# Optimization experiments

Measured on AMD Instinct MI355X. Metric: run time of the kernel, lower is better.

The kernel has to match this reference:

```python
import jax, jax.numpy as jnp
import numpy as np

# Sizes (see shape_source): node irreps 32x0e + 16x1o, edge SH 1x1o,
# messages after concat/filter = 48x0e + 48x1o, MLP 16->64->64->96,
# final equivariant Linear -> 32x0e + 16x1o.
N, E = 50000, 800000
S_IN, V_IN, INV = 32, 16, 16
S_MSG, V_MSG = S_IN + V_IN, S_IN + V_IN  # 48, 48
NFAC = S_MSG + V_MSG                      # 96
S_OUT, V_OUT = 32, 16
SQRT3 = 3.0 ** 0.5


def setup_inputs() -> dict:
    key = jax.random.key(0)
    ks = jax.random.split(key, 12)
    return {
        "edge_src": jax.random.randint(ks[0], (E,), 0, N),
        "edge_dst": jax.random.randint(ks[1], (E,), 0, N),
        "edge_weight_cutoff": jax.random.uniform(ks[2], (E,), dtype=jnp.float32),
        "edge_inv": jax.random.normal(ks[3], (E, INV), dtype=jnp.float32),
        "node_scalars": jax.random.normal(ks[4], (N, S_IN), dtype=jnp.float32),
        "node_vectors": jax.random.normal(ks[5], (N, V_IN, 3), dtype=jnp.float32),
        "edge_sh_vec": jax.random.normal(ks[6], (E, 1, 3), dtype=jnp.float32),
        "W0": jax.random.normal(ks[7], (INV, 64), dtype=jnp.float32),
        "W1": jax.random.normal(ks[8], (64, 64), dtype=jnp.float32),
        "W2": jax.random.normal(ks[9], (64, NFAC), dtype=jnp.float32),
        "WL_s": jax.random.normal(ks[10], (S_MSG, S_OUT), dtype=jnp.float32),
        "WL_v": jax.random.normal(ks[11], (V_MSG, V_OUT), dtype=jnp.float32),
    }


def reference(edge_src, edge_dst, edge_weight_cutoff, edge_inv,
              node_scalars, node_vectors, edge_sh_vec,
              W0, W1, W2, WL_s, WL_v):
    # gather source-node features per edge
    src_s = node_scalars[edge_src]            # [E, 32]
    src_v = node_vectors[edge_src]            # [E, 16, 3]
    ev = edge_sh_vec[:, 0, :]                 # [E, 3] equivariant edge vector (1o)

    # equivariant tensor product (component-normalized CG paths):
    #   0e x 1o -> 1o : scalar * vector
    tp_v = src_s[:, :, None] * edge_sh_vec    # [E, 32, 3]
    #   1o x 1o -> 0e : dot / sqrt(3)   (1e, 2e outputs dropped by the output-irreps filter)
    tp_s = jnp.einsum('eci,ei->ec', src_v, ev) / SQRT3  # [E, 16]

    # concatenate with gathered node features and regroup by irrep
    msg_s = jnp.concatenate([tp_s, src_s], axis=-1)     # [E, 48] (0e block)
    msg_v = jnp.concatenate([tp_v, src_v], axis=1)      # [E, 48, 3] (1o block)

    # edge-conditioned gating MLP on invariant edge features (e3nn-normalized)
    h = jax.nn.silu(edge_inv @ W0 / jnp.sqrt(jnp.float32(INV)))
    h = jax.nn.silu(h @ W1 / jnp.sqrt(jnp.float32(64)))
    fac = h @ W2 / jnp.sqrt(jnp.float32(64))            # [E, 96]

    # elementwise tensor product with scalar factors + smooth cutoff
    g = fac * edge_weight_cutoff[:, None]
    msg_s = msg_s * g[:, :S_MSG]
    msg_v = msg_v * g[:, S_MSG:, None]

    # scatter-sum messages into destination nodes
    out_s = jax.ops.segment_sum(msg_s, edge_dst, num_segments=N)  # [N, 48]
    out_v = jax.ops.segment_sum(msg_v, edge_dst, num_segments=N)  # [N, 48, 3]

    # equivariant Linear to irreps_node_output (fan-in normalized)
    y_s = out_s @ WL_s / jnp.sqrt(jnp.float32(S_MSG))                       # [N, 32]
    y_v = jnp.einsum('eci,co->eoi', out_v, WL_v) / jnp.sqrt(jnp.float32(V_MSG))  # [N, 16, 3]

    # return as contiguous IrrepsArray storage [N, 32 + 16*3]
    return jnp.concatenate([y_s, y_v.reshape(y_v.shape[0], -1)], axis=-1)
```

## Files before the change

kernel.cpp:

```cpp
#include <hip/hip_runtime.h>
#include <hip/hip_fp16.h>
#include <math.h>

constexpr int S_IN = 32, V_IN = 16, INVD = 16;
constexpr int S_MSG = S_IN + V_IN;
constexpr int V_MSG = S_IN + V_IN;
constexpr int NFAC  = S_MSG + V_MSG;
constexpr int S_OUT = 32, V_OUT = 16;
constexpr int OUT_PER_NODE = S_OUT + V_OUT * 3;
constexpr float ISQRT3 = 0.57735026918962576f;
constexpr float ISQ48  = 0.14433756729740643f;

constexpr int PW0 = 0, PW1 = 2560, PW2 = 7168, PWL = 14080, PWTOT = 17536;

typedef _Float16 f16x8 __attribute__((ext_vector_type(8)));
typedef __attribute__((ext_vector_type(4))) float f32x4;

__device__ __forceinline__ float silu_f(float x) {
    return x * __builtin_amdgcn_rcpf(1.0f + __expf(-x));
}
__device__ __forceinline__ unsigned int hpack2(float a, float b) {
    __half2 h = __floats2half2_rn(a, b);
    return *reinterpret_cast<unsigned int*>(&h);
}
__device__ __forceinline__ unsigned short f2h(float f) {
    __half h = __float2half_rn(f);
    return __half_as_ushort(h);
}
__device__ __forceinline__ float h2f(unsigned short u) {
    return __half2float(__ushort_as_half(u));
}
__device__ __forceinline__ float lo16f(unsigned int u) { return h2f((unsigned short)(u & 0xffffu)); }
__device__ __forceinline__ float hi16f(unsigned int u) { return h2f((unsigned short)(u >> 16)); }
__device__ __forceinline__ unsigned int pkmul(unsigned int a, unsigned int b) {
    __half2 ha = *reinterpret_cast<__half2*>(&a);
    __half2 hb = *reinterpret_cast<__half2*>(&b);
    __half2 hc = __hmul2(ha, hb);
    return *reinterpret_cast<unsigned int*>(&hc);
}
__device__ __forceinline__ float2 up2(unsigned int u) {
    __half2 h = *reinterpret_cast<__half2*>(&u);
    return __half22float2(h);
}

__global__ __launch_bounds__(256) void hist_prep(
    const int* __restrict__ edst, int* __restrict__ deg, int E,
    const float* __restrict__ W0, const float* __restrict__ W1,
    const float* __restrict__ W2, const float* __restrict__ WLs,
    const float* __restrict__ WLv,
    const float* __restrict__ ns, const float* __restrict__ nv,
    unsigned short* __restrict__ pW,
    unsigned short* __restrict__ pNS,
    unsigned short* __restrict__ pNV,
    int Nn)
{
    int i = blockIdx.x * 256 + threadIdx.x;
    if (i < E) atomicAdd(&deg[edst[i]], 1);

    int nNS = Nn * 4;
    int nNV = Nn * 6;
    if (i < PWTOT) {
        float v = 0.0f;
        if (i < PW1) {
            int j = i / 40, k = i - 40 * j;
            if (k < INVD) v = W0[k * 64 + j];
        } else if (i < PW2) {
            int t = i - PW1; int j = t / 72, k = t - 72 * j;
            if (k < 64) v = W1[k * 64 + j];
        } else if (i < PWL) {
            int t = i - PW2; int j = t / 72, k = t - 72 * j;
            if (k < 64) v = W2[k * 96 + j];
        } else {
            int t = i - PWL; int j = t / 72, k = t - 72 * j;
            if (k < 48) v = (j < 32) ? WLs[k * S_OUT + j] : WLv[k * V_OUT + (j - 32)];
        }
        pW[i] = f2h(v);
    } else if (i < PWTOT + nNS) {
        int g = i - PWTOT;
        const float4* s4 = reinterpret_cast<const float4*>(ns + (size_t)g * 8);
        float4 a = s4[0], b = s4[1];
        *reinterpret_cast<uint4*>(pNS + (size_t)g * 8) =
            make_uint4(hpack2(a.x, a.y), hpack2(a.z, a.w), hpack2(b.x, b.y), hpack2(b.z, b.w));
    } else if (i < PWTOT + nNS + nNV) {
        int g = i - PWTOT - nNS;
        const float4* s4 = reinterpret_cast<const float4*>(nv + (size_t)g * 8);
        float4 a = s4[0], b = s4[1];
        *reinterpret_cast<uint4*>(pNV + (size_t)g * 8) =
            make_uint4(hpack2(a.x, a.y), hpack2(a.z, a.w), hpack2(b.x, b.y), hpack2(b.z, b.w));
    }
}

__global__ __launch_bounds__(256) void scanA(
    const int* __restrict__ deg, int* __restrict__ bsum, int Nn)
{
    __shared__ int sh[256];
    int i = blockIdx.x * 256 + threadIdx.x;
    sh[threadIdx.x] = (i < Nn) ? deg[i] : 0;
    __syncthreads();
    for (int o = 128; o > 0; o >>= 1) {
        if (threadIdx.x < o) sh[threadIdx.x] += sh[threadIdx.x + o];
        __syncthreads();
    }
    if (threadIdx.x == 0) bsum[blockIdx.x] = sh[0];
}

__global__ __launch_bounds__(1024) void scanB(int* __restrict__ bsum, int nb)
{
    __shared__ int sh[1024];
    int t = threadIdx.x;
    sh[t] = (t < nb) ? bsum[t] : 0;
    __syncthreads();
    for (int o = 1; o < 1024; o <<= 1) {
        int v = (t >= o) ? sh[t - o] : 0;
        __syncthreads();
        sh[t] += v;
        __syncthreads();
    }
    if (t < nb) bsum[t] = (t > 0) ? sh[t - 1] : 0;
}

__global__ __launch_bounds__(256) void scanC(
    const int* __restrict__ deg, const int* __restrict__ bsum,
    int* __restrict__ cursor, int Nn)
{
    __shared__ int sh[256];
    int i = blockIdx.x * 256 + threadIdx.x;
    int t = threadIdx.x;
    int v = (i < Nn) ? deg[i] : 0;
    sh[t] = v;
    __syncthreads();
    for (int o = 1; o < 256; o <<= 1) {
        int u = (t >= o) ? sh[t - o] : 0;
        __syncthreads();
        sh[t] += u;
        __syncthreads();
    }
    int excl = sh[t] - v + bsum[blockIdx.x];
    if (i < Nn) cursor[i] = excl;
}

__global__ __launch_bounds__(256) void scatter_permute(
    const int*   __restrict__ edst,
    const int*   __restrict__ esrc,
    const float* __restrict__ ecut,
    const float* __restrict__ esh,
    const float* __restrict__ einv,
    int* __restrict__ cursor,
    uint4* __restrict__ pedge,
    int E)
{
    int e = blockIdx.x * 256 + threadIdx.x;
    if (e >= E) return;
    int d = edst[e];
    int pos = atomicAdd(&cursor[d], 1);

    const float4* xr = reinterpret_cast<const float4*>(einv + (size_t)e * INVD);
    float4 a = xr[0], b = xr[1], c = xr[2], f = xr[3];
    uint4 r0 = make_uint4(hpack2(a.x, a.y), hpack2(a.z, a.w), hpack2(b.x, b.y), hpack2(b.z, b.w));
    uint4 r1 = make_uint4(hpack2(c.x, c.y), hpack2(c.z, c.w), hpack2(f.x, f.y), hpack2(f.z, f.w));
    uint4 r2 = make_uint4(hpack2(ecut[e], esh[(size_t)e * 3 + 0]),
                          hpack2(esh[(size_t)e * 3 + 1], esh[(size_t)e * 3 + 2]),
                          (unsigned int)esrc[e], (unsigned int)d);

    uint4* dst = pedge + (size_t)pos * 3;
    dst[0] = r0; dst[1] = r1; dst[2] = r2;
}

__global__ __launch_bounds__(256, 5) void edge_mega(
    const uint4* __restrict__ pedge,
    const unsigned short* __restrict__ pW,
    const unsigned short* __restrict__ pNS,
    const unsigned short* __restrict__ pNV,
    float* __restrict__ out,
    int E)
{
    __shared__ __align__(16) unsigned char smem[32768];

    unsigned short* act  = (unsigned short*)(smem + 0);
    unsigned short* sW0T = (unsigned short*)(smem + 18432);
    unsigned short* sW1T = (unsigned short*)(smem + 23552);
    unsigned short* sW2T = (unsigned short*)(smem + 18432);
    unsigned short* sWLT = (unsigned short*)(smem + 18432);
    unsigned short* Fns  = (unsigned short*)(smem + 0);
    unsigned short* Fnv0 = (unsigned short*)(smem + 0);
    unsigned short* Fnv1 = (unsigned short*)(smem + 5120);
    unsigned short* Fnv2 = (unsigned short*)(smem + 10240);
    unsigned short* M    = (unsigned short*)(smem + 0);
    unsigned short* redh = (unsigned short*)(smem + 0);

    const int tid = threadIdx.x;
    const int pbase = blockIdx.x * 128;
    const int p1 = E;

    const int lane = tid & 63;
    const int w    = tid >> 6;
    const int lr   = lane & 15;
    const int lg   = lane >> 4;
    const int eb0  = w * 32 + lr;
    const int eb1  = eb0 + 16;
    const int pA   = pbase + eb0;
    const int pB   = pbase + eb1;

    const uint4 rA2 = pedge[(size_t)(pA < p1 ? pA : p1 - 1) * 3 + 2];
    const uint4 rB2 = pedge[(size_t)(pB < p1 ? pB : p1 - 1) * 3 + 2];
    const float cutA = lo16f(rA2.x);
    const float ev0a = hi16f(rA2.x), ev1a = lo16f(rA2.y), ev2a = hi16f(rA2.y);
    const float cutB = lo16f(rB2.x);
    const float ev0b = hi16f(rB2.x), ev1b = lo16f(rB2.y), ev2b = hi16f(rB2.y);

    const int t2 = tid >> 1, half = tid & 1;
    int dS;
    uint4 pn0, pn1;
    uint4 pv0, pv1, pv2;
    {
        int pS = pbase + t2; if (pS >= p1) pS = p1 - 1;
        uint4 r2 = pedge[(size_t)pS * 3 + 2];
        int sS = (int)r2.z;
        dS = (int)r2.w;
        const uint4* nr = reinterpret_cast<const uint4*>(pNS + (size_t)sS * 32);
        pn0 = nr[half * 2 + 0]; pn1 = nr[half * 2 + 1];
        const uint4* vr = reinterpret_cast<const uint4*>(pNV + (size_t)sS * 48);
        pv0 = vr[half * 3 + 0]; pv1 = vr[half * 3 + 1]; pv2 = vr[half * 3 + 2];
    }

    const uint4* wsrc = reinterpret_cast<const uint4*>(pW);

    {
        uint4* s4 = reinterpret_cast<uint4*>(smem + 18432);
        #pragma unroll 2
        for (int i = tid; i < 896; i += 256) s4[i] = wsrc[i];
    }
    if (tid < 128) {
        int p = pbase + tid; if (p >= p1) p = p1 - 1;
        const uint4* rec = pedge + (size_t)p * 3;
        uint4 r0 = rec[0], r1 = rec[1];
        uint4* r4 = reinterpret_cast<uint4*>(&act[tid * 72]);
        r4[0] = r0;
        r4[1] = r1;
        r4[2] = make_uint4(0u, 0u, 0u, 0u);
        r4[3] = make_uint4(0u, 0u, 0u, 0u);
    }
    __syncthreads();

    const f32x4 zero4 = {0.f, 0.f, 0.f, 0.f};

    {
        f16x8 b0 = *(const f16x8*)&act[eb0 * 72 + lg * 8];
        f16x8 b1 = *(const f16x8*)&act[eb1 * 72 + lg * 8];
        #pragma unroll
        for (int jt = 0; jt < 4; jt++) {
            f16x8 a = *(const f16x8*)&sW0T[(jt * 16 + lr) * 40 + lg * 8];
            f32x4 d0 = __builtin_amdgcn_mfma_f32_16x16x32_f16(a, b0, zero4, 0, 0, 0);
            f32x4 d1 = __builtin_amdgcn_mfma_f32_16x16x32_f16(a, b1, zero4, 0, 0, 0);
            unsigned int u0 = hpack2(silu_f(d0[0] * 0.25f), silu_f(d0[1] * 0.25f));
            unsigned int u1 = hpack2(silu_f(d0[2] * 0.25f), silu_f(d0[3] * 0.25f));
            *(uint2*)&act[eb0 * 72 + jt * 16 + lg * 4] = make_uint2(u0, u1);
            u0 = hpack2(silu_f(d1[0] * 0.25f), silu_f(d1[1] * 0.25f));
            u1 = hpack2(silu_f(d1[2] * 0.25f), silu_f(d1[3] * 0.25f));
            *(uint2*)&act[eb1 * 72 + jt * 16 + lg * 4] = make_uint2(u0, u1);
        }
    }

    {
        f16x8 b00 = *(const f16x8*)&act[eb0 * 72 +      lg * 8];
        f16x8 b01 = *(const f16x8*)&act[eb0 * 72 + 32 + lg * 8];
        f16x8 b10 = *(const f16x8*)&act[eb1 * 72 +      lg * 8];
        f16x8 b11 = *(const f16x8*)&act[eb1 * 72 + 32 + lg * 8];
        #pragma unroll
        for (int jt = 0; jt < 4; jt++) {
            f16x8 a0 = *(const f16x8*)&sW1T[(jt * 16 + lr) * 72 +      lg * 8];
            f16x8 a1 = *(const f16x8*)&sW1T[(jt * 16 + lr) * 72 + 32 + lg * 8];
            f32x4 d0 = __builtin_amdgcn_mfma_f32_16x16x32_f16(a0, b00, zero4, 0, 0, 0);
            d0 = __builtin_amdgcn_mfma_f32_16x16x32_f16(a1, b01, d0, 0, 0, 0);
            f32x4 d1 = __builtin_amdgcn_mfma_f32_16x16x32_f16(a0, b10, zero4, 0, 0, 0);
            d1 = __builtin_amdgcn_mfma_f32_16x16x32_f16(a1, b11, d1, 0, 0, 0);
            unsigned int u0 = hpack2(silu_f(d0[0] * 0.125f), silu_f(d0[1] * 0.125f));
            unsigned int u1 = hpack2(silu_f(d0[2] * 0.125f), silu_f(d0[3] * 0.125f));
            *(uint2*)&act[eb0 * 72 + jt * 16 + lg * 4] = make_uint2(u0, u1);
            u0 = hpack2(silu_f(d1[0] * 0.125f), silu_f(d1[1] * 0.125f));
            u1 = hpack2(silu_f(d1[2] * 0.125f), silu_f(d1[3] * 0.125f));
            *(uint2*)&act[eb1 * 72 + jt * 16 + lg * 4] = make_uint2(u0, u1);
        }
    }

    __syncthreads();
    {
        uint4* a14 = reinterpret_cast<uint4*>(smem + 18432);
        const uint4* w2s = wsrc + 896;
        #pragma unroll 2
        for (int i = tid; i < 864; i += 256) a14[i] = w2s[i];
    }
    __syncthreads();

    float fac0[6][4], fac1[6][4];
    {
        f16x8 b00 = *(const f16x8*)&act[eb0 * 72 +      lg * 8];
        f16x8 b01 = *(const f16x8*)&act[eb0 * 72 + 32 + lg * 8];
        f16x8 b10 = *(const f16x8*)&act[eb1 * 72 +      lg * 8];
        f16x8 b11 = *(const f16x8*)&act[eb1 * 72 + 32 + lg * 8];
        float K0 = cutA * 0.125f * ISQ48;
        float K1 = cutB * 0.125f * ISQ48;
        #pragma unroll
        for (int jt = 0; jt < 6; jt++) {
            f16x8 a0 = *(const f16x8*)&sW2T[(jt * 16 + lr) * 72 +      lg * 8];
            f16x8 a1 = *(const f16x8*)&sW2T[(jt * 16 + lr) * 72 + 32 + lg * 8];
            f32x4 d0 = __builtin_amdgcn_mfma_f32_16x16x32_f16(a0, b00, zero4, 0, 0, 0);
            d0 = __builtin_amdgcn_mfma_f32_16x16x32_f16(a1, b01, d0, 0, 0, 0);
            f32x4 d1 = __builtin_amdgcn_mfma_f32_16x16x32_f16(a0, b10, zero4, 0, 0, 0);
            d1 = __builtin_amdgcn_mfma_f32_16x16x32_f16(a1, b11, d1, 0, 0, 0);
            float s0 = (jt == 0) ? K0 * ISQRT3 : K0;
            float s1 = (jt == 0) ? K1 * ISQRT3 : K1;
            #pragma unroll
            for (int q = 0; q < 4; q++) {
                fac0[jt][q] = d0[q] * s0;
                fac1[jt][q] = d1[q] * s1;
            }
        }
    }
    __syncthreads();

    {
        uint4* wl4 = reinterpret_cast<uint4*>(smem + 18432);
        const uint4* wls = wsrc + 896 + 864;
        #pragma unroll 2
        for (int i = tid; i < 432; i += 256) wl4[i] = wls[i];

        uint4* d4 = reinterpret_cast<uint4*>(&Fns[t2 * 40 + half * 16]);
        d4[0] = pn0; d4[1] = pn1;
    }
    uint2 fsrA[2], fsrB[2];
    #pragma unroll
    for (int jt = 0; jt < 2; jt++) {
        fsrA[jt] = *reinterpret_cast<const uint2*>(&Fns[eb0 * 40 + jt * 16 + lg * 4]);
        fsrB[jt] = *reinterpret_cast<const uint2*>(&Fns[eb1 * 40 + jt * 16 + lg * 4]);
    }
    __syncthreads();

    {
        unsigned int wb[12];
        wb[0]=pv0.x; wb[1]=pv0.y; wb[2]=pv0.z; wb[3]=pv0.w;
        wb[4]=pv1.x; wb[5]=pv1.y; wb[6]=pv1.z; wb[7]=pv1.w;
        wb[8]=pv2.x; wb[9]=pv2.y; wb[10]=pv2.z; wb[11]=pv2.w;
        #pragma unroll
        for (int i = 0; i < 3; i++) {
            unsigned short* FnvI = (i == 0) ? Fnv0 : ((i == 1) ? Fnv1 : Fnv2);
            unsigned int ow[4];
            #pragma unroll
            for (int wd = 0; wd < 4; wd++) {
                int kLo = 6 * wd + i;
                int kHi = 6 * wd + 3 + i;
                unsigned int lo = (kLo & 1) ? (wb[kLo >> 1] >> 16) : (wb[kLo >> 1] & 0xffffu);
                unsigned int hi = (kHi & 1) ? (wb[kHi >> 1] >> 16) : (wb[kHi >> 1] & 0xffffu);
                ow[wd] = lo | (hi << 16);
            }
            uint2* d2 = reinterpret_cast<uint2*>(&FnvI[t2 * 20 + half * 8]);
            d2[0] = make_uint2(ow[0], ow[1]);
            d2[1] = make_uint2(ow[2], ow[3]);
        }
    }
    uint2 fvrA[3], fvrB[3];
    #pragma unroll
    for (int i = 0; i < 3; i++) {
        const unsigned short* FnvI = (i == 0) ? Fnv0 : ((i == 1) ? Fnv1 : Fnv2);
        fvrA[i] = *reinterpret_cast<const uint2*>(&FnvI[eb0 * 20 + lg * 4]);
        fvrB[i] = *reinterpret_cast<const uint2*>(&FnvI[eb1 * 20 + lg * 4]);
    }
    __syncthreads();

    uint2 fpA[5], fpB[5];
    #pragma unroll
    for (int jt = 1; jt < 6; jt++) {
        fpA[jt - 1] = make_uint2(hpack2(fac0[jt][0], fac0[jt][1]), hpack2(fac0[jt][2], fac0[jt][3]));
        fpB[jt - 1] = make_uint2(hpack2(fac1[jt][0], fac1[jt][1]), hpack2(fac1[jt][2], fac1[jt][3]));
    }

    {
        float2 a0 = up2(fvrA[0].x), a1 = up2(fvrA[0].y);
        float2 b0 = up2(fvrA[1].x), b1 = up2(fvrA[1].y);
        float2 c0 = up2(fvrA[2].x), c1 = up2(fvrA[2].y);
        float2 d0 = up2(fvrB[0].x), d1 = up2(fvrB[0].y);
        float2 e0 = up2(fvrB[1].x), e1 = up2(fvrB[1].y);
        float2 g0 = up2(fvrB[2].x), g1 = up2(fvrB[2].y);
        float vA[4], vB[4];
        vA[0] = (a0.x*ev0a + b0.x*ev1a + c0.x*ev2a) * fac0[0][0];
        vA[1] = (a0.y*ev0a + b0.y*ev1a + c0.y*ev2a) * fac0[0][1];
        vA[2] = (a1.x*ev0a + b1.x*ev1a + c1.x*ev2a) * fac0[0][2];
        vA[3] = (a1.y*ev0a + b1.y*ev1a + c1.y*ev2a) * fac0[0][3];
        vB[0] = (d0.x*ev0b + e0.x*ev1b + g0.x*ev2b) * fac1[0][0];
        vB[1] = (d0.y*ev0b + e0.y*ev1b + g0.y*ev2b) * fac1[0][1];
        vB[2] = (d1.x*ev0b + e1.x*ev1b + g1.x*ev2b) * fac1[0][2];
        vB[3] = (d1.y*ev0b + e1.y*ev1b + g1.y*ev2b) * fac1[0][3];
        *(uint2*)&M[eb0 * 72 + lg * 4] = make_uint2(hpack2(vA[0], vA[1]), hpack2(vA[2], vA[3]));
        *(uint2*)&M[eb1 * 72 + lg * 4] = make_uint2(hpack2(vB[0], vB[1]), hpack2(vB[2], vB[3]));
    }
    #pragma unroll
    for (int jt = 1; jt < 3; jt++) {
        int c0 = jt * 16 + lg * 4;
        *(uint2*)&M[eb0 * 72 + c0] =
            make_uint2(pkmul(fsrA[jt-1].x, fpA[jt-1].x), pkmul(fsrA[jt-1].y, fpA[jt-1].y));
        *(uint2*)&M[eb1 * 72 + c0] =
            make_uint2(pkmul(fsrB[jt-1].x, fpB[jt-1].x), pkmul(fsrB[jt-1].y, fpB[jt-1].y));
    }
    *(uint2*)&M[eb0 * 72 + 48 + lg * 4] = make_uint2(0u, 0u);
    *(uint2*)&M[eb1 * 72 + 48 + lg * 4] = make_uint2(0u, 0u);

    f32x4 accS[2][2] = {{zero4, zero4}, {zero4, zero4}};
    #pragma unroll
    for (int kt = 0; kt < 2; kt++) {
        f16x8 b0 = *(const f16x8*)&M[eb0 * 72 + kt * 32 + lg * 8];
        f16x8 b1 = *(const f16x8*)&M[eb1 * 72 + kt * 32 + lg * 8];
        #pragma unroll
        for (int ot = 0; ot < 2; ot++) {
            f16x8 a = *(const f16x8*)&sWLT[(ot * 16 + lr) * 72 + kt * 32 + lg * 8];
            accS[0][ot] = __builtin_amdgcn_mfma_f32_16x16x32_f16(a, b0, accS[0][ot], 0, 0, 0);
            accS[1][ot] = __builtin_amdgcn_mfma_f32_16x16x32_f16(a, b1, accS[1][ot], 0, 0, 0);
        }
    }

    #pragma unroll
    for (int jt = 0; jt < 2; jt++) {
        int c0 = jt * 16 + lg * 4;
        *(uint2*)&M[eb0 * 72 + c0] =
            make_uint2(pkmul(fsrA[jt].x, fpA[jt+2].x), pkmul(fsrA[jt].y, fpA[jt+2].y));
        *(uint2*)&M[eb1 * 72 + c0] =
            make_uint2(pkmul(fsrB[jt].x, fpB[jt+2].x), pkmul(fsrB[jt].y, fpB[jt+2].y));
    }
    f32x4 t1A = zero4, t1B = zero4;
    {
        f16x8 b0 = *(const f16x8*)&M[eb0 * 72 + lg * 8];
        f16x8 b1 = *(const f16x8*)&M[eb1 * 72 + lg * 8];
        f16x8 a  = *(const f16x8*)&sWLT[(32 + lr) * 72 + lg * 8];
        t1A = __builtin_amdgcn_mfma_f32_16x16x32_f16(a, b0, t1A, 0, 0, 0);
        t1B = __builtin_amdgcn_mfma_f32_16x16x32_f16(a, b1, t1B, 0, 0, 0);
    }

    float yvA[4][3], yvB[4][3];
    *(uint2*)&M[eb0 * 72 + 16 + lg * 4] = make_uint2(0u, 0u);
    *(uint2*)&M[eb1 * 72 + 16 + lg * 4] = make_uint2(0u, 0u);
    #pragma unroll
    for (int i = 0; i < 3; i++) {
        *(uint2*)&M[eb0 * 72 + lg * 4] =
            make_uint2(pkmul(fvrA[i].x, fpA[4].x), pkmul(fvrA[i].y, fpA[4].y));
        *(uint2*)&M[eb1 * 72 + lg * 4] =
            make_uint2(pkmul(fvrB[i].x, fpB[4].x), pkmul(fvrB[i].y, fpB[4].y));

        f32x4 t2A = zero4, t2B = zero4;
        f16x8 b0 = *(const f16x8*)&M[eb0 * 72 + lg * 8];
        f16x8 b1 = *(const f16x8*)&M[eb1 * 72 + lg * 8];
        f16x8 a  = *(const f16x8*)&sWLT[(32 + lr) * 72 + 32 + lg * 8];
        t2A = __builtin_amdgcn_mfma_f32_16x16x32_f16(a, b0, t2A, 0, 0, 0);
        t2B = __builtin_amdgcn_mfma_f32_16x16x32_f16(a, b1, t2B, 0, 0, 0);

        float evA = (i == 0) ? ev0a : ((i == 1) ? ev1a : ev2a);
        float evB = (i == 0) ? ev0b : ((i == 1) ? ev1b : ev2b);
        #pragma unroll
        for (int q = 0; q < 4; q++) {
            yvA[q][i] = fmaf(evA, t1A[q], t2A[q]);
            yvB[q][i] = fmaf(evB, t1B[q], t2B[q]);
        }
    }

    __syncthreads();

    {
        bool okA = (pA < p1), okB = (pB < p1);
        #pragma unroll
        for (int ot = 0; ot < 2; ot++) {
            f32x4 sA = okA ? accS[0][ot] : zero4;
            f32x4 sB = okB ? accS[1][ot] : zero4;
            *(uint2*)&redh[eb0 * 84 + ot * 16 + lg * 4] =
                make_uint2(hpack2(sA[0], sA[1]), hpack2(sA[2], sA[3]));
            *(uint2*)&redh[eb1 * 84 + ot * 16 + lg * 4] =
                make_uint2(hpack2(sB[0], sB[1]), hpack2(sB[2], sB[3]));
        }
        float zA[12], zB[12];
        #pragma unroll
        for (int q = 0; q < 4; q++)
            #pragma unroll
            for (int i = 0; i < 3; i++) {
                zA[3*q+i] = okA ? yvA[q][i] : 0.0f;
                zB[3*q+i] = okB ? yvB[q][i] : 0.0f;
            }
        uint2* dA = (uint2*)&redh[eb0 * 84 + 32 + 12 * lg];
        dA[0] = make_uint2(hpack2(zA[0], zA[1]),  hpack2(zA[2], zA[3]));
        dA[1] = make_uint2(hpack2(zA[4], zA[5]),  hpack2(zA[6], zA[7]));
        dA[2] = make_uint2(hpack2(zA[8], zA[9]),  hpack2(zA[10], zA[11]));
        uint2* dB = (uint2*)&redh[eb1 * 84 + 32 + 12 * lg];
        dB[0] = make_uint2(hpack2(zB[0], zB[1]),  hpack2(zB[2], zB[3]));
        dB[1] = make_uint2(hpack2(zB[4], zB[5]),  hpack2(zB[6], zB[7]));
        dB[2] = make_uint2(hpack2(zB[8], zB[9]),  hpack2(zB[10], zB[11]));
    }

    {
        int base = w * 32;
        int cur = __shfl(dS, 0);
        float s0 = 0.0f, s1 = 0.0f;
        for (int r = 0; r < 32; r++) {
            int d = __shfl(dS, 2 * r);
            if (d != cur) {
                atomicAdd(&out[(size_t)cur * OUT_PER_NODE + lane], s0);
                if (lane < 16) atomicAdd(&out[(size_t)cur * OUT_PER_NODE + 64 + lane], s1);
                s0 = 0.0f; s1 = 0.0f; cur = d;
            }
            const unsigned short* row = &redh[(base + r) * 84];
            s0 += h2f(row[lane]);
            if (lane < 16) s1 += h2f(row[64 + lane]);
        }
        atomicAdd(&out[(size_t)cur * OUT_PER_NODE + lane], s0);
        if (lane < 16) atomicAdd(&out[(size_t)cur * OUT_PER_NODE + 64 + lane], s1);
    }
}

extern "C" void kernel_launch(void* const* d_in, const int* in_sizes, int n_in,
                              void* d_out, int out_size, void* d_ws, size_t ws_size,
                              hipStream_t stream) {
    const int*   esrc = (const int*)  d_in[0];
    const int*   edst = (const int*)  d_in[1];
    const float* ecut = (const float*)d_in[2];
    const float* einv = (const float*)d_in[3];
    const float* ns   = (const float*)d_in[4];
    const float* nv   = (const float*)d_in[5];
    const float* esh  = (const float*)d_in[6];
    const float* W0   = (const float*)d_in[7];
    const float* W1   = (const float*)d_in[8];
    const float* W2   = (const float*)d_in[9];
    const float* WLs  = (const float*)d_in[10];
    const float* WLv  = (const float*)d_in[11];
    float* out = (float*)d_out;

    const int E  = in_sizes[0];
    const int Nn = in_sizes[4] / S_IN;
    const int nb = (Nn + 255) / 256;

    size_t int_bytes = (((size_t)(2 * Nn + nb)) * sizeof(int) + 255) & ~(size_t)255;
    size_t pe_bytes  = ((size_t)E * 48 + 255) & ~(size_t)255;
    size_t pw_bytes  = ((size_t)PWTOT * 2 + 255) & ~(size_t)255;
    size_t ns_bytes  = ((size_t)Nn * 32 * 2 + 255) & ~(size_t)255;
    size_t nv_bytes  = ((size_t)Nn * 48 * 2 + 255) & ~(size_t)255;
    size_t fixed = int_bytes + pe_bytes + pw_bytes + ns_bytes + nv_bytes;

    int eblocks = (E + 255) / 256;

    hipMemsetAsync(out, 0, (size_t)Nn * OUT_PER_NODE * sizeof(float), stream);

    if (ws_size < fixed) return;

    int*            deg    = (int*)d_ws;
    int*            cursor = deg + Nn;
    int*            bsum   = cursor + Nn;
    uint4*          pedge  = (uint4*)((char*)d_ws + int_bytes);
    unsigned short* pW     = (unsigned short*)((char*)d_ws + int_bytes + pe_bytes);
    unsigned short* pNS    = (unsigned short*)((char*)d_ws + int_bytes + pe_bytes + pw_bytes);
    unsigned short* pNV    = (unsigned short*)((char*)d_ws + int_bytes + pe_bytes + pw_bytes + ns_bytes);

    hipMemsetAsync(deg, 0, (size_t)Nn * sizeof(int), stream);

    int ptotal = PWTOT + Nn * 4 + Nn * 6;
    int hp_blocks = max(eblocks, (ptotal + 255) / 256);
    hist_prep<<<hp_blocks, 256, 0, stream>>>(edst, deg, E, W0, W1, W2, WLs, WLv,
                                             ns, nv, pW, pNS, pNV, Nn);
    scanA<<<nb, 256, 0, stream>>>(deg, bsum, Nn);
    scanB<<<1, 1024, 0, stream>>>(bsum, nb);
    scanC<<<nb, 256, 0, stream>>>(deg, bsum, cursor, Nn);
    scatter_permute<<<eblocks, 256, 0, stream>>>(edst, esrc, ecut, esh, einv,
                                                 cursor, pedge, E);

    int mblocks = (E + 127) / 128;
    edge_mega<<<mblocks, 256, 0, stream>>>(pedge, pW, pNS, pNV, out, E);
}
```

Before: 217.4 us.

## Merge three-pass scan into single-block scan and split node-feature staging by thread half

Replaces the three-kernel exclusive scan over node degrees with one 1024-thread block in which each thread serially sums a contiguous chunk, then does a block scan and writes the offsets. This removes two kernel launches and the intermediate block-sum buffer, at the cost of strided, poorly coalesced serial loops over about 50 per-thread entries. In edge_mega, the shared-memory layout is rearranged so scalar and vector features of gathered nodes live in separate regions. One thread of each pair loads the scalars and the other the vectors, which removes one __syncthreads between staging phases; a barrier is added before the final reduction instead.

```diff
diff --git a/kernel.cpp b/kernel.cpp
--- a/kernel.cpp
+++ b/kernel.cpp
@@ -90,53 +90,30 @@
     }
 }
 
-__global__ __launch_bounds__(256) void scanA(
-    const int* __restrict__ deg, int* __restrict__ bsum, int Nn)
+__global__ __launch_bounds__(1024) void scan1(
+    const int* __restrict__ deg, int* __restrict__ cursor, int Nn)
 {
-    __shared__ int sh[256];
-    int i = blockIdx.x * 256 + threadIdx.x;
-    sh[threadIdx.x] = (i < Nn) ? deg[i] : 0;
-    __syncthreads();
-    for (int o = 128; o > 0; o >>= 1) {
-        if (threadIdx.x < o) sh[threadIdx.x] += sh[threadIdx.x + o];
+    const int T = 1024;
+    int t = threadIdx.x;
+    int chunk = (Nn + T - 1) / T;
+    int lo = t * chunk;
+    int hi = lo + chunk; if (hi > Nn) hi = Nn;
+    int s = 0;
+    for (int i = lo; i < hi; i++) s += deg[i];
+    __shared__ int ps[T];
+    ps[t] = s;
+    __syncthreads();
+    for (int off = 1; off < T; off <<= 1) {
+        int v = (t >= off) ? ps[t - off] : 0;
         __syncthreads();
-    }
-    if (threadIdx.x == 0) bsum[blockIdx.x] = sh[0];
-}
-
-__global__ __launch_bounds__(1024) void scanB(int* __restrict__ bsum, int nb)
-{
-    __shared__ int sh[1024];
-    int t = threadIdx.x;
-    sh[t] = (t < nb) ? bsum[t] : 0;
-    __syncthreads();
-    for (int o = 1; o < 1024; o <<= 1) {
-        int v = (t >= o) ? sh[t - o] : 0;
+        ps[t] += v;
         __syncthreads();
-        sh[t] += v;
-        __syncthreads();
-    }
-    if (t < nb) bsum[t] = (t > 0) ? sh[t - 1] : 0;
-}
-
-__global__ __launch_bounds__(256) void scanC(
-    const int* __restrict__ deg, const int* __restrict__ bsum,
-    int* __restrict__ cursor, int Nn)
-{
-    __shared__ int sh[256];
-    int i = blockIdx.x * 256 + threadIdx.x;
-    int t = threadIdx.x;
-    int v = (i < Nn) ? deg[i] : 0;
-    sh[t] = v;
-    __syncthreads();
-    for (int o = 1; o < 256; o <<= 1) {
-        int u = (t >= o) ? sh[t - o] : 0;
-        __syncthreads();
-        sh[t] += u;
-        __syncthreads();
-    }
-    int excl = sh[t] - v + bsum[blockIdx.x];
-    if (i < Nn) cursor[i] = excl;
+    }
+    int base = (t > 0) ? ps[t - 1] : 0;
+    for (int i = lo; i < hi; i++) {
+        cursor[i] = base;
+        base += deg[i];
+    }
 }
 
 __global__ __launch_bounds__(256) void scatter_permute(
@@ -180,12 +157,12 @@
     unsigned short* sW0T = (unsigned short*)(smem + 18432);
     unsigned short* sW1T = (unsigned short*)(smem + 23552);
     unsigned short* sW2T = (unsigned short*)(smem + 18432);
-    unsigned short* sWLT = (unsigned short*)(smem + 18432);
-    unsigned short* Fns  = (unsigned short*)(smem + 0);
-    unsigned short* Fnv0 = (unsigned short*)(smem + 0);
-    unsigned short* Fnv1 = (unsigned short*)(smem + 5120);
-    unsigned short* Fnv2 = (unsigned short*)(smem + 10240);
-    unsigned short* M    = (unsigned short*)(smem + 0);
+    unsigned short* sWLT = (unsigned short*)(smem + 0);
+    unsigned short* Fns  = (unsigned short*)(smem + 6912);
+    unsigned short* Fnv0 = (unsigned short*)(smem + 17152);
+    unsigned short* Fnv1 = (unsigned short*)(smem + 22272);
+    unsigned short* Fnv2 = (unsigned short*)(smem + 27392);
+    unsigned short* M    = (unsigned short*)(smem + 6912);
     unsigned short* redh = (unsigned short*)(smem + 0);
 
     const int tid = threadIdx.x;
@@ -210,17 +187,19 @@
 
     const int t2 = tid >> 1, half = tid & 1;
     int dS;
-    uint4 pn0, pn1;
-    uint4 pv0, pv1, pv2;
+    uint4 pf0, pf1, pf2, pf3, pf4, pf5;
     {
         int pS = pbase + t2; if (pS >= p1) pS = p1 - 1;
         uint4 r2 = pedge[(size_t)pS * 3 + 2];
         int sS = (int)r2.z;
         dS = (int)r2.w;
-        const uint4* nr = reinterpret_cast<const uint4*>(pNS + (size_t)sS * 32);
-        pn0 = nr[half * 2 + 0]; pn1 = nr[half * 2 + 1];
-        const uint4* vr = reinterpret_cast<const uint4*>(pNV + (size_t)sS * 48);
-        pv0 = vr[half * 3 + 0]; pv1 = vr[half * 3 + 1]; pv2 = vr[half * 3 + 2];
+        if (half == 0) {
+            const uint4* nr = reinterpret_cast<const uint4*>(pNS + (size_t)sS * 32);
+            pf0 = nr[0]; pf1 = nr[1]; pf2 = nr[2]; pf3 = nr[3];
+        } else {
+            const uint4* vr = reinterpret_cast<const uint4*>(pNV + (size_t)sS * 48);
+            pf0 = vr[0]; pf1 = vr[1]; pf2 = vr[2]; pf3 = vr[3]; pf4 = vr[4]; pf5 = vr[5];
+        }
     }
 
     const uint4* wsrc = reinterpret_cast<const uint4*>(pW);
@@ -320,45 +299,50 @@
     __syncthreads();
 
     {
-        uint4* wl4 = reinterpret_cast<uint4*>(smem + 18432);
+        uint4* wl4 = reinterpret_cast<uint4*>(smem);
         const uint4* wls = wsrc + 896 + 864;
         #pragma unroll 2
         for (int i = tid; i < 432; i += 256) wl4[i] = wls[i];
 
-        uint4* d4 = reinterpret_cast<uint4*>(&Fns[t2 * 40 + half * 16]);
-        d4[0] = pn0; d4[1] = pn1;
-    }
-    uint2 fsrA[2], fsrB[2];
+        if (half == 0) {
+            uint4* d4 = reinterpret_cast<uint4*>(&Fns[t2 * 40]);
+            d4[0] = pf0; d4[1] = pf1;
+            uint4* d4b = reinterpret_cast<uint4*>(&Fns[t2 * 40 + 16]);
+            d4b[0] = pf2; d4b[1] = pf3;
+        } else {
+            unsigned int wb[24];
+            wb[0]=pf0.x; wb[1]=pf0.y; wb[2]=pf0.z; wb[3]=pf0.w;
+            wb[4]=pf1.x; wb[5]=pf1.y; wb[6]=pf1.z; wb[7]=pf1.w;
+            wb[8]=pf2.x; wb[9]=pf2.y; wb[10]=pf2.z; wb[11]=pf2.w;
+            wb[12]=pf3.x; wb[13]=pf3.y; wb[14]=pf3.z; wb[15]=pf3.w;
+            wb[16]=pf4.x; wb[17]=pf4.y; wb[18]=pf4.z; wb[19]=pf4.w;
+            wb[20]=pf5.x; wb[21]=pf5.y; wb[22]=pf5.z; wb[23]=pf5.w;
+            #pragma unroll
+            for (int i = 0; i < 3; i++) {
+                unsigned short* FnvI = (i == 0) ? Fnv0 : ((i == 1) ? Fnv1 : Fnv2);
+                unsigned int ow[8];
+                #pragma unroll
+                for (int wd = 0; wd < 8; wd++) {
+                    int kLo = 6 * wd + i;
+                    int kHi = 6 * wd + 3 + i;
+                    unsigned int lo = (kLo & 1) ? (wb[kLo >> 1] >> 16) : (wb[kLo >> 1] & 0xffffu);
+                    unsigned int hi = (kHi & 1) ? (wb[kHi >> 1] >> 16) : (wb[kHi >> 1] & 0xffffu);
+                    ow[wd] = lo | (hi << 16);
+                }
+                uint2* d2 = reinterpret_cast<uint2*>(&FnvI[t2 * 20]);
+                d2[0] = make_uint2(ow[0], ow[1]);
+                d2[1] = make_uint2(ow[2], ow[3]);
+                d2[2] = make_uint2(ow[4], ow[5]);
+                d2[3] = make_uint2(ow[6], ow[7]);
+            }
+        }
+    }
+    uint2 fsrA[2], fsrB[2], fvrA[3], fvrB[3];
     #pragma unroll
     for (int jt = 0; jt < 2; jt++) {
         fsrA[jt] = *reinterpret_cast<const uint2*>(&Fns[eb0 * 40 + jt * 16 + lg * 4]);
         fsrB[jt] = *reinterpret_cast<const uint2*>(&Fns[eb1 * 40 + jt * 16 + lg * 4]);
     }
-    __syncthreads();
-
-    {
-        unsigned int wb[12];
-        wb[0]=pv0.x; wb[1]=pv0.y; wb[2]=pv0.z; wb[3]=pv0.w;
-        wb[4]=pv1.x; wb[5]=pv1.y; wb[6]=pv1.z; wb[7]=pv1.w;
-        wb[8]=pv2.x; wb[9]=pv2.y; wb[10]=pv2.z; wb[11]=pv2.w;
-        #pragma unroll
-        for (int i = 0; i < 3; i++) {
-            unsigned short* FnvI = (i == 0) ? Fnv0 : ((i == 1) ? Fnv1 : Fnv2);
-            unsigned int ow[4];
-            #pragma unroll
-            for (int wd = 0; wd < 4; wd++) {
-                int kLo = 6 * wd + i;
-                int kHi = 6 * wd + 3 + i;
-                unsigned int lo = (kLo & 1) ? (wb[kLo >> 1] >> 16) : (wb[kLo >> 1] & 0xffffu);
-                unsigned int hi = (kHi & 1) ? (wb[kHi >> 1] >> 16) : (wb[kHi >> 1] & 0xffffu);
-                ow[wd] = lo | (hi << 16);
-            }
-            uint2* d2 = reinterpret_cast<uint2*>(&FnvI[t2 * 20 + half * 8]);
-            d2[0] = make_uint2(ow[0], ow[1]);
-            d2[1] = make_uint2(ow[2], ow[3]);
-        }
-    }
-    uint2 fvrA[3], fvrB[3];
     #pragma unroll
     for (int i = 0; i < 3; i++) {
         const unsigned short* FnvI = (i == 0) ? Fnv0 : ((i == 1) ? Fnv1 : Fnv2);
@@ -490,6 +474,7 @@
         dB[1] = make_uint2(hpack2(zB[4], zB[5]),  hpack2(zB[6], zB[7]));
         dB[2] = make_uint2(hpack2(zB[8], zB[9]),  hpack2(zB[10], zB[11]));
     }
+    __syncthreads();
 
     {
         int base = w * 32;
@@ -530,9 +515,8 @@
 
     const int E  = in_sizes[0];
     const int Nn = in_sizes[4] / S_IN;
-    const int nb = (Nn + 255) / 256;
-
-    size_t int_bytes = (((size_t)(2 * Nn + nb)) * sizeof(int) + 255) & ~(size_t)255;
+
+    size_t int_bytes = (((size_t)(2 * Nn)) * sizeof(int) + 255) & ~(size_t)255;
     size_t pe_bytes  = ((size_t)E * 48 + 255) & ~(size_t)255;
     size_t pw_bytes  = ((size_t)PWTOT * 2 + 255) & ~(size_t)255;
     size_t ns_bytes  = ((size_t)Nn * 32 * 2 + 255) & ~(size_t)255;
@@ -547,7 +531,6 @@
 
     int*            deg    = (int*)d_ws;
     int*            cursor = deg + Nn;
-    int*            bsum   = cursor + Nn;
     uint4*          pedge  = (uint4*)((char*)d_ws + int_bytes);
     unsigned short* pW     = (unsigned short*)((char*)d_ws + int_bytes + pe_bytes);
     unsigned short* pNS    = (unsigned short*)((char*)d_ws + int_bytes + pe_bytes + pw_bytes);
@@ -559,9 +542,7 @@
     int hp_blocks = max(eblocks, (ptotal + 255) / 256);
     hist_prep<<<hp_blocks, 256, 0, stream>>>(edst, deg, E, W0, W1, W2, WLs, WLv,
                                              ns, nv, pW, pNS, pNV, Nn);
-    scanA<<<nb, 256, 0, stream>>>(deg, bsum, Nn);
-    scanB<<<1, 1024, 0, stream>>>(bsum, nb);
-    scanC<<<nb, 256, 0, stream>>>(deg, bsum, cursor, Nn);
+    scan1<<<1, 1024, 0, stream>>>(deg, cursor, Nn);
     scatter_permute<<<eblocks, 256, 0, stream>>>(edst, esrc, ecut, esh, einv,
                                                  cursor, pedge, E);
 
```

Measured after the change: 269.5 us. 1.24x slower.
